# Kernel optimization log

Hardware: AMD Instinct MI355X
Metric: run time of the kernel (lower is better)

## Reference

```python
import jax, jax.numpy as jnp
import numpy as np

B, L, IN_DIM, D, NL, DI, DS, DC, DTR, V, TRM_LOOPS = 4, 2048, 480, 512, 8, 1024, 16, 4, 32, 21, 4
EPS = 1e-5


def _ln(x, g, b):
    mu = jnp.mean(x, axis=-1, keepdims=True)
    var = jnp.mean(jnp.square(x - mu), axis=-1, keepdims=True)
    return (x - mu) * jax.lax.rsqrt(var + EPS) * g + b


def setup_inputs() -> dict:
    key = jax.random.key(0)
    ks = iter(jax.random.split(key, 48))
    n = lambda shape, s=0.02: jax.random.normal(next(ks), shape, jnp.float32) * s
    return dict(
        x=jax.random.normal(next(ks), (B, L, IN_DIM), jnp.float32),
        enc_w1=n((D, IN_DIM)), enc_b1=jnp.zeros((D,), jnp.float32),
        enc_w2=n((D, D)), enc_b2=jnp.zeros((D,), jnp.float32),
        enc_g=jnp.ones((D,), jnp.float32), enc_beta=jnp.zeros((D,), jnp.float32),
        gru_wih=n((3 * D, D)), gru_whh=n((3 * D, D)),
        gru_bih=jnp.zeros((3 * D,), jnp.float32), gru_bhh=jnp.zeros((3 * D,), jnp.float32),
        prj_w1=n((D, D)), prj_b1=jnp.zeros((D,), jnp.float32),
        prj_w2=n((D, D)), prj_b2=jnp.zeros((D,), jnp.float32),
        trm_g=jnp.ones((D,), jnp.float32), trm_beta=jnp.zeros((D,), jnp.float32),
        in_w=n((NL, 2 * DI, D)),
        conv_w=n((NL, DI, 1, DC), 0.2), conv_b=jnp.zeros((NL, DI), jnp.float32),
        xproj_w=n((NL, DTR + 2 * DS, DI)),
        dt_w=n((NL, DI, DTR), 0.1), dt_b=n((NL, DI), 0.1),
        A_log=jnp.log(jnp.broadcast_to(jnp.arange(1, DS + 1, dtype=jnp.float32), (NL, DI, DS))),
        Dp=jnp.ones((NL, DI), jnp.float32),
        out_w=n((NL, D, DI)),
        ln_g=jnp.ones((NL, D), jnp.float32), ln_b=jnp.zeros((NL, D), jnp.float32),
        head_w=n((V, D)), head_b=jnp.zeros((V,), jnp.float32),
    )


def _mamba(x, in_w, conv_w, conv_b, xproj_w, dt_w, dt_b, A_log, Dp, out_w):
    # x: [B,L,D]
    xz = jnp.einsum('bld,ed->ble', x, in_w)          # [B,L,2*DI]
    xi, zgate = jnp.split(xz, 2, axis=-1)
    # depthwise causal conv over time
    xc = jnp.transpose(xi, (0, 2, 1))                # [B,DI,L]
    xc = jax.lax.conv_general_dilated(
        xc, conv_w, (1,), [(DC - 1, 0)], feature_group_count=DI,
        dimension_numbers=('NCH', 'OIH', 'NCH'))
    xc = jax.nn.silu(jnp.transpose(xc, (0, 2, 1)) + conv_b)   # [B,L,DI]
    dbl = jnp.einsum('bld,ed->ble', xc, xproj_w)     # [B,L,DTR+2*DS]
    dt = dbl[..., :DTR]
    Bm = dbl[..., DTR:DTR + DS]
    Cm = dbl[..., DTR + DS:]
    dt = jax.nn.softplus(jnp.einsum('blr,dr->bld', dt, dt_w) + dt_b)  # [B,L,DI]
    A = -jnp.exp(A_log)                              # [DI,DS]

    def step(h, ins):
        dt_t, B_t, C_t, x_t = ins                    # [B,DI],[B,DS],[B,DS],[B,DI]
        dA = jnp.exp(dt_t[:, :, None] * A)           # [B,DI,DS]
        h = dA * h + (dt_t * x_t)[:, :, None] * B_t[:, None, :]
        y = jnp.einsum('bds,bs->bd', h, C_t)
        return h, y

    h0 = jnp.zeros((x.shape[0], DI, DS), x.dtype)
    xs = (jnp.swapaxes(dt, 0, 1), jnp.swapaxes(Bm, 0, 1),
          jnp.swapaxes(Cm, 0, 1), jnp.swapaxes(xc, 0, 1))
    _, ys = jax.lax.scan(step, h0, xs)               # ys: [L,B,DI]
    y = jnp.swapaxes(ys, 0, 1) + xc * Dp
    y = y * jax.nn.silu(zgate)
    return jnp.einsum('ble,de->bld', y, out_w)


def reference(x, enc_w1, enc_b1, enc_w2, enc_b2, enc_g, enc_beta,
              gru_wih, gru_whh, gru_bih, gru_bhh,
              prj_w1, prj_b1, prj_w2, prj_b2, trm_g, trm_beta,
              in_w, conv_w, conv_b, xproj_w, dt_w, dt_b, A_log, Dp, out_w,
              ln_g, ln_b, head_w, head_b):
    # encoder
    h = jax.nn.gelu(x @ enc_w1.T + enc_b1, approximate=False)
    h = _ln(h @ enc_w2.T + enc_b2, enc_g, enc_beta)
    # TRM refinement
    b, l, d = h.shape
    xf = h.reshape(-1, d)
    z = jnp.zeros_like(xf)
    for _ in range(TRM_LOOPS):
        gi = xf @ gru_wih.T + gru_bih
        gh = z @ gru_whh.T + gru_bhh
        ir, iz, inn = jnp.split(gi, 3, axis=-1)
        hr, hz, hn = jnp.split(gh, 3, axis=-1)
        r = jax.nn.sigmoid(ir + hr)
        u = jax.nn.sigmoid(iz + hz)
        nn_ = jnp.tanh(inn + r * hn)
        z = (1.0 - u) * nn_ + u * z
        delta = jax.nn.gelu(z @ prj_w1.T + prj_b1, approximate=False) @ prj_w2.T + prj_b2
        xf = xf + delta
    h = _ln(xf, trm_g, trm_beta).reshape(b, l, d)
    # stacked Mamba blocks with post-norm residual
    for i in range(NL):
        h = _ln(h + _mamba(h, in_w[i], conv_w[i], conv_b[i], xproj_w[i],
                           dt_w[i], dt_b[i], A_log[i], Dp[i], out_w[i]),
                ln_g[i], ln_b[i])
    return h @ head_w.T + head_b
```

## Files before the change

kernel.cpp:

```cpp
#include <hip/hip_runtime.h>
#include <hip/hip_bf16.h>
#include <math.h>

#define BB 4
#define LL 2048
#define IN_DIM 480
#define DD 512
#define NLAYER 8
#define DI 1024
#define DS 16
#define DC 4
#define DTR 32
#define VV 21
#define TRM_LOOPS 4
#define ROWS (BB*LL)
#define EPSLN 1e-5f

#define NCHUNK 128
#define CLEN (LL / NCHUNK)

#define ACT_NONE 0
#define ACT_GELU 1
#define ACT_SOFTPLUS 2

typedef __attribute__((ext_vector_type(8))) short short8v;
typedef __attribute__((ext_vector_type(4))) float f32x4;

__device__ __forceinline__ float softplus_fast(float x) {
  return (x > 20.f) ? x : __logf(1.f + __expf(x));
}
__device__ __forceinline__ float bf2f(__hip_bfloat16 v) { return __bfloat162float(v); }

template<int ACT, bool RES, bool WF32, bool WBF16>
__global__ __launch_bounds__(256)
void gemm_mfma_bt(const __hip_bfloat16* __restrict__ A,
                  const __hip_bfloat16* __restrict__ B,
                  const float* __restrict__ bias,
                  const float* __restrict__ res,
                  float* __restrict__ Cf, __hip_bfloat16* __restrict__ Cb,
                  int M, int N, int K) {
  __shared__ short As[128 * 32];
  __shared__ short Bs[128 * 32];
  const int tid = threadIdx.x;
  const int lane = tid & 63;
  const int wv = tid >> 6;
  const int wr = (wv >> 1) * 64;
  const int wc = (wv & 1) * 64;
  const int fr = lane & 15;
  const int ko = (lane >> 4) * 8;

  int bid = blockIdx.y * gridDim.x + blockIdx.x;
  const int nwg = gridDim.x * gridDim.y;
  if ((nwg & 7) == 0) {
    bid = (bid & 7) * (nwg >> 3) + (bid >> 3);
  }
  const int m0 = (bid / gridDim.x) * 128;
  const int n0 = (bid % gridDim.x) * 128;

  f32x4 acc[4][4];
  #pragma unroll
  for (int i = 0; i < 4; ++i)
    #pragma unroll
    for (int j = 0; j < 4; ++j)
      acc[i][j] = (f32x4){0.f, 0.f, 0.f, 0.f};

  for (int k0 = 0; k0 < K; k0 += 32) {
    #pragma unroll
    for (int jj = 0; jj < 2; ++jj) {
      const int chunk = jj * 256 + tid;
      const int r = chunk >> 2;
      const int cb = (chunk & 3) * 8;
      const __hip_bfloat16* ga = A + (size_t)(m0 + r) * K + k0 + cb;
      __builtin_amdgcn_global_load_lds(
          (const __attribute__((address_space(1))) unsigned int*)ga,
          (__attribute__((address_space(3))) unsigned int*)&As[chunk * 8], 16, 0, 0);
      const __hip_bfloat16* gb = B + (size_t)(n0 + r) * K + k0 + cb;
      __builtin_amdgcn_global_load_lds(
          (const __attribute__((address_space(1))) unsigned int*)gb,
          (__attribute__((address_space(3))) unsigned int*)&Bs[chunk * 8], 16, 0, 0);
    }
    __syncthreads();

    short8v a[4], b[4];
    #pragma unroll
    for (int i = 0; i < 4; ++i)
      a[i] = *(const short8v*)&As[(wr + i * 16 + fr) * 32 + ko];
    #pragma unroll
    for (int j = 0; j < 4; ++j)
      b[j] = *(const short8v*)&Bs[(wc + j * 16 + fr) * 32 + ko];
    #pragma unroll
    for (int i = 0; i < 4; ++i)
      #pragma unroll
      for (int j = 0; j < 4; ++j)
        acc[i][j] = __builtin_amdgcn_mfma_f32_16x16x32_bf16(a[i], b[j], acc[i][j], 0, 0, 0);
    __syncthreads();
  }

  float bj[4];
  #pragma unroll
  for (int j = 0; j < 4; ++j)
    bj[j] = bias ? bias[n0 + wc + j * 16 + fr] : 0.f;
  const int r0 = (lane >> 4) * 4;
  #pragma unroll
  for (int i = 0; i < 4; ++i) {
    #pragma unroll
    for (int r = 0; r < 4; ++r) {
      const int row = m0 + wr + i * 16 + r0 + r;
      const size_t rb = (size_t)row * N;
      #pragma unroll
      for (int j = 0; j < 4; ++j) {
        const int col = n0 + wc + j * 16 + fr;
        float v = acc[i][j][r] + bj[j];
        if (ACT == ACT_GELU) v = 0.5f * v * (1.0f + erff(v * 0.70710678118654752f));
        if (ACT == ACT_SOFTPLUS) v = softplus_fast(v);
        if (RES) v += res[rb + col];
        if (WF32) Cf[rb + col] = v;
        if (WBF16) Cb[rb + col] = __float2bfloat16(v);
      }
    }
  }
}

template<bool ATOMIC, bool BIASF>
__global__ __launch_bounds__(256)
void gemm_mfma_n64(const __hip_bfloat16* __restrict__ A,
                   const __hip_bfloat16* __restrict__ B,
                   const float* __restrict__ bias,
                   float* __restrict__ C,
                   int M, int K, int klen, int nout, int ldc) {
  __shared__ short As[64 * 32];
  __shared__ short Bs[64 * 32];
  const int tid = threadIdx.x;
  const int lane = tid & 63;
  const int wv = tid >> 6;
  const int wr = (wv >> 1) * 32;
  const int wc = (wv & 1) * 32;
  const int fr = lane & 15;
  const int ko = (lane >> 4) * 8;
  const int m0 = blockIdx.y * 64;
  const int kbase = blockIdx.x * klen;

  f32x4 acc[2][2];
  #pragma unroll
  for (int i = 0; i < 2; ++i)
    #pragma unroll
    for (int j = 0; j < 2; ++j)
      acc[i][j] = (f32x4){0.f, 0.f, 0.f, 0.f};

  for (int k0 = kbase; k0 < kbase + klen; k0 += 32) {
    const int r = tid >> 2;
    const int cb = (tid & 3) * 8;
    const __hip_bfloat16* ga = A + (size_t)(m0 + r) * K + k0 + cb;
    __builtin_amdgcn_global_load_lds(
        (const __attribute__((address_space(1))) unsigned int*)ga,
        (__attribute__((address_space(3))) unsigned int*)&As[tid * 8], 16, 0, 0);
    const __hip_bfloat16* gb = B + (size_t)r * K + k0 + cb;
    __builtin_amdgcn_global_load_lds(
        (const __attribute__((address_space(1))) unsigned int*)gb,
        (__attribute__((address_space(3))) unsigned int*)&Bs[tid * 8], 16, 0, 0);
    __syncthreads();

    short8v a[2], b[2];
    #pragma unroll
    for (int i = 0; i < 2; ++i)
      a[i] = *(const short8v*)&As[(wr + i * 16 + fr) * 32 + ko];
    #pragma unroll
    for (int j = 0; j < 2; ++j)
      b[j] = *(const short8v*)&Bs[(wc + j * 16 + fr) * 32 + ko];
    #pragma unroll
    for (int i = 0; i < 2; ++i)
      #pragma unroll
      for (int j = 0; j < 2; ++j)
        acc[i][j] = __builtin_amdgcn_mfma_f32_16x16x32_bf16(a[i], b[j], acc[i][j], 0, 0, 0);
    __syncthreads();
  }

  const int r0 = (lane >> 4) * 4;
  #pragma unroll
  for (int i = 0; i < 2; ++i) {
    #pragma unroll
    for (int r = 0; r < 4; ++r) {
      const int row = m0 + wr + i * 16 + r0 + r;
      const size_t rb = (size_t)row * ldc;
      #pragma unroll
      for (int j = 0; j < 2; ++j) {
        const int col = wc + j * 16 + fr;
        float v = acc[i][j][r];
        if (ATOMIC) {
          atomicAdd(&C[rb + col], v);
        } else {
          if (col < nout) {
            if (BIASF) v += bias[col];
            C[rb + col] = v;
          }
        }
      }
    }
  }
}

__global__ __launch_bounds__(256)
void cvt_f2b(const float* __restrict__ s, __hip_bfloat16* __restrict__ d, int n) {
  int i = (blockIdx.x * 256 + threadIdx.x) * 4;
  if (i >= n) return;
  float4 v = *(const float4*)(s + i);
  d[i + 0] = __float2bfloat16(v.x);
  d[i + 1] = __float2bfloat16(v.y);
  d[i + 2] = __float2bfloat16(v.z);
  d[i + 3] = __float2bfloat16(v.w);
}

__global__ __launch_bounds__(256)
void cvt_dbl32(const float* __restrict__ dbl, __hip_bfloat16* __restrict__ o) {
  int i = blockIdx.x * 256 + threadIdx.x;
  if (i >= ROWS * 8) return;
  int row = i >> 3, q = (i & 7) * 4;
  float4 v = *(const float4*)(dbl + (size_t)row * 64 + q);
  short4 p;
  short* pp = (short*)&p;
  __hip_bfloat16 b0 = __float2bfloat16(v.x); pp[0] = *(short*)&b0;
  __hip_bfloat16 b1 = __float2bfloat16(v.y); pp[1] = *(short*)&b1;
  __hip_bfloat16 b2 = __float2bfloat16(v.z); pp[2] = *(short*)&b2;
  __hip_bfloat16 b3 = __float2bfloat16(v.w); pp[3] = *(short*)&b3;
  *(short4*)(o + (size_t)row * 32 + q) = p;
}

template<bool XF32>
__global__ __launch_bounds__(256)
void ln_kernel(const void* __restrict__ xv, const float* __restrict__ res,
               const float* __restrict__ g, const float* __restrict__ b,
               float* __restrict__ outf, __hip_bfloat16* __restrict__ outb) {
  const int row = blockIdx.x;
  const int t = threadIdx.x;
  const size_t base = (size_t)row * DD;
  float v0, v1;
  if (XF32) {
    const float* x = (const float*)xv;
    v0 = x[base + t]; v1 = x[base + t + 256];
  } else {
    const __hip_bfloat16* x = (const __hip_bfloat16*)xv;
    v0 = bf2f(x[base + t]); v1 = bf2f(x[base + t + 256]);
  }
  if (res) { v0 += res[base + t]; v1 += res[base + t + 256]; }
  float s  = v0 + v1;
  float ss = v0 * v0 + v1 * v1;
  #pragma unroll
  for (int off = 32; off > 0; off >>= 1) {
    s  += __shfl_down(s, off);
    ss += __shfl_down(ss, off);
  }
  __shared__ float red[2][4];
  int wave = t >> 6, lane = t & 63;
  if (lane == 0) { red[0][wave] = s; red[1][wave] = ss; }
  __syncthreads();
  if (t == 0) {
    float S = red[0][0] + red[0][1] + red[0][2] + red[0][3];
    float SS = red[1][0] + red[1][1] + red[1][2] + red[1][3];
    red[0][0] = S; red[1][0] = SS;
  }
  __syncthreads();
  float mean = red[0][0] * (1.f / DD);
  float var  = red[1][0] * (1.f / DD) - mean * mean;
  float inv  = rsqrtf(var + EPSLN);
  float o0 = (v0 - mean) * inv * g[t]       + b[t];
  float o1 = (v1 - mean) * inv * g[t + 256] + b[t + 256];
  outf[base + t]       = o0;
  outf[base + t + 256] = o1;
  outb[base + t]       = __float2bfloat16(o0);
  outb[base + t + 256] = __float2bfloat16(o1);
}

__device__ __forceinline__ float fsig(float x) { return 1.f / (1.f + __expf(-x)); }
__device__ __forceinline__ void bf4_load(const __hip_bfloat16* p, float* f) {
  short4 v = *(const short4*)p;
  f[0] = __uint_as_float(((unsigned)(unsigned short)v.x) << 16);
  f[1] = __uint_as_float(((unsigned)(unsigned short)v.y) << 16);
  f[2] = __uint_as_float(((unsigned)(unsigned short)v.z) << 16);
  f[3] = __uint_as_float(((unsigned)(unsigned short)v.w) << 16);
}

__global__ __launch_bounds__(256)
void gru_gates(const __hip_bfloat16* __restrict__ gi, const __hip_bfloat16* __restrict__ gh,
               float* __restrict__ z, __hip_bfloat16* __restrict__ zbf) {
  int idx4 = blockIdx.x * 256 + threadIdx.x;
  if (idx4 >= ROWS * DD / 4) return;
  const int m = idx4 >> 7;
  const int n = (idx4 & 127) * 4;
  const size_t base = (size_t)m * (3 * DD);
  float ir[4], iz[4], in_[4], hr[4], hz[4], hn[4];
  bf4_load(gi + base + n, ir);
  bf4_load(gi + base + 512 + n, iz);
  bf4_load(gi + base + 1024 + n, in_);
  bf4_load(gh + base + n, hr);
  bf4_load(gh + base + 512 + n, hz);
  bf4_load(gh + base + 1024 + n, hn);
  const size_t zo_i = (size_t)m * DD + n;
  float4 zov = *(const float4*)(z + zo_i);
  float zo[4] = {zov.x, zov.y, zov.z, zov.w};
  float zn[4];
  short4 ob;
  short* op = (short*)&ob;
  #pragma unroll
  for (int j = 0; j < 4; ++j) {
    float rg = fsig(ir[j] + hr[j]);
    float ug = fsig(iz[j] + hz[j]);
    float xx = in_[j] + rg * hn[j];
    xx = fminf(fmaxf(xx, -9.f), 9.f);
    float t2 = __expf(2.f * xx);
    float nn = (t2 - 1.f) / (t2 + 1.f);
    zn[j] = (1.f - ug) * nn + ug * zo[j];
    __hip_bfloat16 hb = __float2bfloat16(zn[j]);
    op[j] = *reinterpret_cast<short*>(&hb);
  }
  *(float4*)(z + zo_i) = make_float4(zn[0], zn[1], zn[2], zn[3]);
  *(short4*)(zbf + zo_i) = ob;
}

__global__ __launch_bounds__(256)
void conv_silu(const __hip_bfloat16* __restrict__ xz, const float* __restrict__ w,
               const float* __restrict__ cb, __hip_bfloat16* __restrict__ xc) {
  int idx4 = blockIdx.x * 256 + threadIdx.x;
  if (idx4 >= ROWS * DI / 4) return;
  const int d0 = (idx4 << 2) & (DI - 1);
  const int bl = idx4 >> 8;
  const int l = bl & (LL - 1);
  const __hip_bfloat16* xp = xz + (size_t)bl * (2 * DI) + d0;
  float t0[4] = {0,0,0,0}, t1[4] = {0,0,0,0}, t2[4] = {0,0,0,0}, t3[4];
  bf4_load(xp, t3);
  if (l >= 1) bf4_load(xp - (ptrdiff_t)(1 * 2 * DI), t2);
  if (l >= 2) bf4_load(xp - (ptrdiff_t)(2 * 2 * DI), t1);
  if (l >= 3) bf4_load(xp - (ptrdiff_t)(3 * 2 * DI), t0);
  float4 cbv = *(const float4*)(cb + d0);
  float cb4[4] = {cbv.x, cbv.y, cbv.z, cbv.w};
  short4 o;
  short* op = (short*)&o;
  #pragma unroll
  for (int j = 0; j < 4; ++j) {
    float4 wv = *(const float4*)(w + (d0 + j) * 4);
    float acc = cb4[j];
    acc = fmaf(wv.x, t0[j], acc);
    acc = fmaf(wv.y, t1[j], acc);
    acc = fmaf(wv.z, t2[j], acc);
    acc = fmaf(wv.w, t3[j], acc);
    float r = acc / (1.f + __expf(-acc));
    __hip_bfloat16 hb = __float2bfloat16(r);
    op[j] = *reinterpret_cast<short*>(&hb);
  }
  *(short4*)(xc + (size_t)bl * DI + d0) = o;
}


__global__ __launch_bounds__(256)
void scan_pass1(const __hip_bfloat16* __restrict__ xc, const float* __restrict__ dbl,
                const float* __restrict__ A_log, const __hip_bfloat16* __restrict__ dt,
                __hip_bfloat16* __restrict__ hF, float* __restrict__ dtsum) {
  __shared__ float sB[CLEN][DS];
  const int tid = threadIdx.x;
  const int d = (blockIdx.x & 3) * 256 + tid;
  const int c = (blockIdx.x >> 2) & (NCHUNK - 1);
  const int b = (int)(blockIdx.x >> 9);
  const size_t row0 = (size_t)b * LL + (size_t)c * CLEN;
  if (tid < CLEN * DS / 4) {
    const int r = tid >> 2, q = (tid & 3) * 4;
    float4 v = *(const float4*)(dbl + (row0 + r) * 64 + DTR + q);
    *(float4*)&sB[r][q] = v;
  }
  __syncthreads();

  const float A0 = -__expf(A_log[(size_t)d * DS]);
  float h[DS];
  #pragma unroll
  for (int s = 0; s < DS; ++s) h[s] = 0.f;
  float dts = 0.f;

  for (int l = 0; l < CLEN; ++l) {
    const size_t rk = row0 + l;
    float dtv = bf2f(dt[rk * DI + d]);
    dts += dtv;
    float xv = bf2f(xc[rk * DI + d]);
    float du = dtv * xv;
    float e1 = __expf(dtv * A0);
    float a = 1.f;
    #pragma unroll
    for (int s4 = 0; s4 < DS; s4 += 4) {
      float4 Bv = *(const float4*)&sB[l][s4];
      a *= e1; h[s4+0] = fmaf(a, h[s4+0], du * Bv.x);
      a *= e1; h[s4+1] = fmaf(a, h[s4+1], du * Bv.y);
      a *= e1; h[s4+2] = fmaf(a, h[s4+2], du * Bv.z);
      a *= e1; h[s4+3] = fmaf(a, h[s4+3], du * Bv.w);
    }
  }
  const size_t o = ((size_t)(b * NCHUNK + c) * DI + d) * DS;
  short4 pk[4];
  #pragma unroll
  for (int s4 = 0; s4 < DS; s4 += 4) {
    short* pp = (short*)&pk[s4 >> 2];
    #pragma unroll
    for (int j = 0; j < 4; ++j) {
      __hip_bfloat16 hb = __float2bfloat16(h[s4 + j]);
      pp[j] = *reinterpret_cast<short*>(&hb);
    }
    *(short4*)(hF + o + s4) = pk[s4 >> 2];
  }
  dtsum[(size_t)(b * NCHUNK + c) * DI + d] = dts;
}

__global__ __launch_bounds__(256)
void scan_pass2(const float* __restrict__ A_log, const float* __restrict__ dtsum,
                __hip_bfloat16* __restrict__ hF) {
  const int idx = blockIdx.x * 256 + threadIdx.x;
  const int s = idx & (DS - 1);
  const int d = (idx >> 4) & (DI - 1);
  const int b = idx >> 14;
  const float A = -__expf(A_log[d * DS + s]);
  float h = 0.f;
  for (int c = 0; c < NCHUNK; ++c) {
    const size_t cb = (size_t)(b * NCHUNK + c) * DI + d;
    const float p = __expf(dtsum[cb] * A);
    const size_t o = cb * DS + s;
    const float hf = bf2f(hF[o]);
    hF[o] = __float2bfloat16(h);
    h = fmaf(p, h, hf);
  }
}

__global__ __launch_bounds__(256)
void scan_pass3(const __hip_bfloat16* __restrict__ xc, const float* __restrict__ dbl,
                const float* __restrict__ A_log, const __hip_bfloat16* __restrict__ dt,
                const __hip_bfloat16* __restrict__ hin, const __hip_bfloat16* __restrict__ xz,
                const float* __restrict__ Dp, __hip_bfloat16* __restrict__ y) {
  __shared__ float sbc[CLEN][32];
  const int tid = threadIdx.x;
  const int d = (blockIdx.x & 3) * 256 + tid;
  const int c = (blockIdx.x >> 2) & (NCHUNK - 1);
  const int b = (int)(blockIdx.x >> 9);
  const size_t row0 = (size_t)b * LL + (size_t)c * CLEN;
  if (tid < CLEN * 32 / 4) {
    const int r = tid >> 3, q = (tid & 7) * 4;
    float4 v = *(const float4*)(dbl + (row0 + r) * 64 + DTR + q);
    *(float4*)&sbc[r][q] = v;
  }
  __syncthreads();

  const float A0 = -__expf(A_log[(size_t)d * DS]);
  float h[DS];
  const size_t o = ((size_t)(b * NCHUNK + c) * DI + d) * DS;
  #pragma unroll
  for (int s4 = 0; s4 < DS; s4 += 4) {
    float hv[4];
    bf4_load(hin + o + s4, hv);
    h[s4] = hv[0]; h[s4+1] = hv[1]; h[s4+2] = hv[2]; h[s4+3] = hv[3];
  }
  const float Dval = Dp[d];

  for (int l = 0; l < CLEN; ++l) {
    const size_t rk = row0 + l;
    float dtv = bf2f(dt[rk * DI + d]);
    float xv = bf2f(xc[rk * DI + d]);
    float du = dtv * xv;
    float e1 = __expf(dtv * A0);
    float a = 1.f;
    float acc = 0.f;
    #pragma unroll
    for (int s4 = 0; s4 < DS; s4 += 4) {
      float4 Bv = *(const float4*)&sbc[l][s4];
      float4 Cv = *(const float4*)&sbc[l][16 + s4];
      a *= e1; h[s4+0] = fmaf(a, h[s4+0], du * Bv.x); acc = fmaf(h[s4+0], Cv.x, acc);
      a *= e1; h[s4+1] = fmaf(a, h[s4+1], du * Bv.y); acc = fmaf(h[s4+1], Cv.y, acc);
      a *= e1; h[s4+2] = fmaf(a, h[s4+2], du * Bv.z); acc = fmaf(h[s4+2], Cv.z, acc);
      a *= e1; h[s4+3] = fmaf(a, h[s4+3], du * Bv.w); acc = fmaf(h[s4+3], Cv.w, acc);
    }
    float zg = bf2f(xz[rk * 2 * DI + DI + d]);
    float sz = zg / (1.f + __expf(-zg));
    y[rk * DI + d] = __float2bfloat16(fmaf(xv, Dval, acc) * sz);
  }
}

extern "C" void kernel_launch(void* const* d_in, const int* in_sizes, int n_in,
                              void* d_out, int out_size, void* d_ws, size_t ws_size,
                              hipStream_t stream) {
  (void)in_sizes; (void)n_in; (void)out_size; (void)ws_size;
  const float* x       = (const float*)d_in[0];
  const float* enc_w1  = (const float*)d_in[1];
  const float* enc_b1  = (const float*)d_in[2];
  const float* enc_w2  = (const float*)d_in[3];
  const float* enc_b2  = (const float*)d_in[4];
  const float* enc_g   = (const float*)d_in[5];
  const float* enc_beta= (const float*)d_in[6];
  const float* gru_wih = (const float*)d_in[7];
  const float* gru_whh = (const float*)d_in[8];
  const float* gru_bih = (const float*)d_in[9];
  const float* gru_bhh = (const float*)d_in[10];
  const float* prj_w1  = (const float*)d_in[11];
  const float* prj_b1  = (const float*)d_in[12];
  const float* prj_w2  = (const float*)d_in[13];
  const float* prj_b2  = (const float*)d_in[14];
  const float* trm_g   = (const float*)d_in[15];
  const float* trm_beta= (const float*)d_in[16];
  const float* in_w    = (const float*)d_in[17];
  const float* conv_w  = (const float*)d_in[18];
  const float* conv_b  = (const float*)d_in[19];
  const float* xproj_w = (const float*)d_in[20];
  const float* dt_w    = (const float*)d_in[21];
  const float* dt_b    = (const float*)d_in[22];
  const float* A_log   = (const float*)d_in[23];
  const float* Dp      = (const float*)d_in[24];
  const float* out_w   = (const float*)d_in[25];
  const float* ln_g    = (const float*)d_in[26];
  const float* ln_b    = (const float*)d_in[27];
  const float* head_w  = (const float*)d_in[28];
  const float* head_b  = (const float*)d_in[29];
  float* out = (float*)d_out;

  float* ws = (float*)d_ws;
  float* h     = ws + 0;
  __hip_bfloat16* hbf   = (__hip_bfloat16*)(ws + 4194304);
  __hip_bfloat16* wenc1 = (__hip_bfloat16*)(ws + 6291456);
  __hip_bfloat16* wenc2 = (__hip_bfloat16*)(ws + 6414336);
  __hip_bfloat16* wgih  = (__hip_bfloat16*)(ws + 6545408);
  __hip_bfloat16* wghh  = (__hip_bfloat16*)(ws + 6938624);
  __hip_bfloat16* wp1   = (__hip_bfloat16*)(ws + 7331840);
  __hip_bfloat16* wp2   = (__hip_bfloat16*)(ws + 7462912);
  __hip_bfloat16* win   = (__hip_bfloat16*)(ws + 7593984);
  __hip_bfloat16* wout  = (__hip_bfloat16*)(ws + 11788288);
  __hip_bfloat16* wxp   = (__hip_bfloat16*)(ws + 13885440);
  __hip_bfloat16* whead = (__hip_bfloat16*)(ws + 14147584);
  __hip_bfloat16* wdtb  = (__hip_bfloat16*)(ws + 14163968);
  float* p0 = ws + 14295040;
  __hip_bfloat16* tmpb2 = (__hip_bfloat16*)p0;
  __hip_bfloat16* xbf   = (__hip_bfloat16*)(p0 + 4194304);
  __hip_bfloat16* tmpbf = (__hip_bfloat16*)(p0 + 31457280);
  float* z  = p0;
  __hip_bfloat16* zbf = (__hip_bfloat16*)(p0 + 4194304);
  __hip_bfloat16* gib = (__hip_bfloat16*)(p0 + 6291456);
  __hip_bfloat16* ghb = (__hip_bfloat16*)(p0 + 12582912);
  __hip_bfloat16* xzbf = (__hip_bfloat16*)p0;
  __hip_bfloat16* xcbf = (__hip_bfloat16*)(p0 + 8388608);
  float* dbl = p0 + 12582912;
  __hip_bfloat16* ybbf = (__hip_bfloat16*)(p0 + 13107200);
  __hip_bfloat16* hFb  = (__hip_bfloat16*)(p0 + 17301504);
  float* dts = p0 + 21495808;
  __hip_bfloat16* dtb16 = (__hip_bfloat16*)(p0 + 22020096);
  __hip_bfloat16* dblb  = (__hip_bfloat16*)(p0 + 26214400);
  __hip_bfloat16* tmpob = (__hip_bfloat16*)(p0 + 26345472);

  dim3 b256(256);
  dim3 gG((ROWS * DD / 4 + 255) / 256), gLN(ROWS);
  dim3 gConv((ROWS * DI / 4 + 255) / 256);
  dim3 gScan(BB * NCHUNK * (DI / 256));
  dim3 gScan2(BB * DI * DS / 256);

  {
    auto cvt = [&](const float* s, __hip_bfloat16* d, int n) {
      hipLaunchKernelGGL(cvt_f2b, dim3((n / 4 + 255) / 256), b256, 0, stream, s, d, n);
    };
    cvt(x, xbf, ROWS * IN_DIM);
    cvt(enc_w1, wenc1, DD * IN_DIM);
    cvt(enc_w2, wenc2, DD * DD);
    cvt(gru_wih, wgih, 3 * DD * DD);
    cvt(gru_whh, wghh, 3 * DD * DD);
    cvt(prj_w1, wp1, DD * DD);
    cvt(prj_w2, wp2, DD * DD);
    cvt(in_w, win, NLAYER * 2 * DI * DD);
    cvt(out_w, wout, NLAYER * DD * DI);
    cvt(xproj_w, wxp, NLAYER * 64 * DI);
    cvt(dt_w, wdtb, NLAYER * DI * DTR);
    hipMemsetAsync(whead, 0, 64 * DD * sizeof(__hip_bfloat16), stream);
    cvt(head_w, whead, VV * DD);
  }

  hipLaunchKernelGGL((gemm_mfma_bt<ACT_GELU, false, false, true>), dim3(DD/128, ROWS/128), b256, 0, stream,
                     xbf, wenc1, enc_b1, nullptr, nullptr, tmpbf, ROWS, DD, IN_DIM);
  hipLaunchKernelGGL((gemm_mfma_bt<ACT_NONE, false, false, true>), dim3(DD/128, ROWS/128), b256, 0, stream,
                     tmpbf, wenc2, enc_b2, nullptr, nullptr, tmpb2, ROWS, DD, DD);
  hipLaunchKernelGGL((ln_kernel<false>), gLN, b256, 0, stream, tmpb2, (const float*)nullptr, enc_g, enc_beta, h, hbf);

  hipMemsetAsync(z, 0, (size_t)ROWS * DD * sizeof(float), stream);
  hipMemsetAsync(zbf, 0, (size_t)ROWS * DD * sizeof(__hip_bfloat16), stream);
  for (int it = 0; it < TRM_LOOPS; ++it) {
    hipLaunchKernelGGL((gemm_mfma_bt<ACT_NONE, false, false, true>), dim3(3*DD/128, ROWS/128), b256, 0, stream,
                       hbf, wgih, gru_bih, nullptr, nullptr, gib, ROWS, 3 * DD, DD);
    hipLaunchKernelGGL((gemm_mfma_bt<ACT_NONE, false, false, true>), dim3(3*DD/128, ROWS/128), b256, 0, stream,
                       zbf, wghh, gru_bhh, nullptr, nullptr, ghb, ROWS, 3 * DD, DD);
    hipLaunchKernelGGL(gru_gates, gG, b256, 0, stream, gib, ghb, z, zbf);
    hipLaunchKernelGGL((gemm_mfma_bt<ACT_GELU, false, false, true>), dim3(DD/128, ROWS/128), b256, 0, stream,
                       zbf, wp1, prj_b1, nullptr, nullptr, tmpbf, ROWS, DD, DD);
    hipLaunchKernelGGL((gemm_mfma_bt<ACT_NONE, true, true, true>), dim3(DD/128, ROWS/128), b256, 0, stream,
                       tmpbf, wp2, prj_b2, h, h, hbf, ROWS, DD, DD);
  }
  hipLaunchKernelGGL((ln_kernel<true>), gLN, b256, 0, stream, h, (const float*)nullptr, trm_g, trm_beta, h, hbf);

  for (int i = 0; i < NLAYER; ++i) {
    const __hip_bfloat16* iw  = win  + (size_t)i * 2 * DI * DD;
    const __hip_bfloat16* ow  = wout + (size_t)i * DD * DI;
    const __hip_bfloat16* xpw = wxp  + (size_t)i * 64 * DI;
    const __hip_bfloat16* dwb = wdtb + (size_t)i * DI * DTR;
    const float* cw  = conv_w  + (size_t)i * DI * DC;
    const float* cbi = conv_b  + (size_t)i * DI;
    const float* db  = dt_b    + (size_t)i * DI;
    const float* Al  = A_log   + (size_t)i * DI * DS;
    const float* Dpi = Dp      + (size_t)i * DI;
    const float* lgi = ln_g    + (size_t)i * DD;
    const float* lbi = ln_b    + (size_t)i * DD;

    hipLaunchKernelGGL((gemm_mfma_bt<ACT_NONE, false, false, true>), dim3(2*DI/128, ROWS/128), b256, 0, stream,
                       hbf, iw, nullptr, nullptr, nullptr, xzbf, ROWS, 2 * DI, DD);
    hipLaunchKernelGGL(conv_silu, gConv, b256, 0, stream, xzbf, cw, cbi, xcbf);
    hipMemsetAsync(dbl, 0, (size_t)ROWS * 64 * sizeof(float), stream);
    hipLaunchKernelGGL((gemm_mfma_n64<true, false>), dim3(2, ROWS / 64), b256, 0, stream,
                       xcbf, xpw, nullptr, dbl, ROWS, DI, DI / 2, 64, 64);
    hipLaunchKernelGGL(cvt_dbl32, dim3(ROWS * 8 / 256), b256, 0, stream, dbl, dblb);
    hipLaunchKernelGGL((gemm_mfma_bt<ACT_SOFTPLUS, false, false, true>), dim3(DI/128, ROWS/128), b256, 0, stream,
                       dblb, dwb, db, nullptr, nullptr, dtb16, ROWS, DI, DTR);
    hipLaunchKernelGGL(scan_pass1, gScan, b256, 0, stream, xcbf, dbl, Al, dtb16, hFb, dts);
    hipLaunchKernelGGL(scan_pass2, gScan2, b256, 0, stream, Al, dts, hFb);
    hipLaunchKernelGGL(scan_pass3, gScan, b256, 0, stream, xcbf, dbl, Al, dtb16, hFb, xzbf, Dpi, ybbf);
    hipLaunchKernelGGL((gemm_mfma_bt<ACT_NONE, false, false, true>), dim3(DD/128, ROWS/128), b256, 0, stream,
                       ybbf, ow, nullptr, nullptr, nullptr, tmpob, ROWS, DD, DI);
    hipLaunchKernelGGL((ln_kernel<false>), gLN, b256, 0, stream, tmpob, h, lgi, lbi, h, hbf);
  }

  hipLaunchKernelGGL((gemm_mfma_n64<false, true>), dim3(1, ROWS / 64), b256, 0, stream,
                     hbf, whead, head_b, out, ROWS, DD, DD, VV, VV);
}
```

Measured before the change: 1.818 ms.

## Skip first GRU hidden GEMM, fuse dbl zeroing, prefetch scan loads

On the first TRM iteration z is zero, so the hidden-state GEMM is replaced by loading the bias directly in a specialised gru_gates kernel. The fp32 z buffer is dropped and the recurrent state is kept only in bf16, which removes the memsets and the fp32 traffic but rounds the GRU state each iteration. The per-layer memset of dbl is folded into conv_silu. The scan kernels software-prefetch the next row's x, dt and gate values to hide load latency.

```diff
diff --git a/kernel.cpp b/kernel.cpp
--- a/kernel.cpp
+++ b/kernel.cpp
@@ -279,9 +279,10 @@
   f[3] = __uint_as_float(((unsigned)(unsigned short)v.w) << 16);
 }
 
+template<bool FIRST>
 __global__ __launch_bounds__(256)
 void gru_gates(const __hip_bfloat16* __restrict__ gi, const __hip_bfloat16* __restrict__ gh,
-               float* __restrict__ z, __hip_bfloat16* __restrict__ zbf) {
+               const float* __restrict__ bhh, __hip_bfloat16* __restrict__ zbf) {
   int idx4 = blockIdx.x * 256 + threadIdx.x;
   if (idx4 >= ROWS * DD / 4) return;
   const int m = idx4 >> 7;
@@ -291,13 +292,21 @@
   bf4_load(gi + base + n, ir);
   bf4_load(gi + base + 512 + n, iz);
   bf4_load(gi + base + 1024 + n, in_);
-  bf4_load(gh + base + n, hr);
-  bf4_load(gh + base + 512 + n, hz);
-  bf4_load(gh + base + 1024 + n, hn);
+  if (FIRST) {
+    float4 a = *(const float4*)(bhh + n);
+    float4 bq = *(const float4*)(bhh + 512 + n);
+    float4 cq = *(const float4*)(bhh + 1024 + n);
+    hr[0]=a.x; hr[1]=a.y; hr[2]=a.z; hr[3]=a.w;
+    hz[0]=bq.x; hz[1]=bq.y; hz[2]=bq.z; hz[3]=bq.w;
+    hn[0]=cq.x; hn[1]=cq.y; hn[2]=cq.z; hn[3]=cq.w;
+  } else {
+    bf4_load(gh + base + n, hr);
+    bf4_load(gh + base + 512 + n, hz);
+    bf4_load(gh + base + 1024 + n, hn);
+  }
   const size_t zo_i = (size_t)m * DD + n;
-  float4 zov = *(const float4*)(z + zo_i);
-  float zo[4] = {zov.x, zov.y, zov.z, zov.w};
-  float zn[4];
+  float zo[4] = {0.f, 0.f, 0.f, 0.f};
+  if (!FIRST) bf4_load(zbf + zo_i, zo);
   short4 ob;
   short* op = (short*)&ob;
   #pragma unroll
@@ -308,19 +317,22 @@
     xx = fminf(fmaxf(xx, -9.f), 9.f);
     float t2 = __expf(2.f * xx);
     float nn = (t2 - 1.f) / (t2 + 1.f);
-    zn[j] = (1.f - ug) * nn + ug * zo[j];
-    __hip_bfloat16 hb = __float2bfloat16(zn[j]);
+    float zn = FIRST ? (1.f - ug) * nn : ((1.f - ug) * nn + ug * zo[j]);
+    __hip_bfloat16 hb = __float2bfloat16(zn);
     op[j] = *reinterpret_cast<short*>(&hb);
   }
-  *(float4*)(z + zo_i) = make_float4(zn[0], zn[1], zn[2], zn[3]);
   *(short4*)(zbf + zo_i) = ob;
 }
 
 __global__ __launch_bounds__(256)
 void conv_silu(const __hip_bfloat16* __restrict__ xz, const float* __restrict__ w,
-               const float* __restrict__ cb, __hip_bfloat16* __restrict__ xc) {
+               const float* __restrict__ cb, __hip_bfloat16* __restrict__ xc,
+               float* __restrict__ dbl_zero) {
   int idx4 = blockIdx.x * 256 + threadIdx.x;
   if (idx4 >= ROWS * DI / 4) return;
+  if (idx4 < ROWS * 64 / 4) {
+    *(float4*)(dbl_zero + (size_t)idx4 * 4) = make_float4(0.f, 0.f, 0.f, 0.f);
+  }
   const int d0 = (idx4 << 2) & (DI - 1);
   const int bl = idx4 >> 8;
   const int l = bl & (LL - 1);
@@ -373,11 +385,18 @@
   for (int s = 0; s < DS; ++s) h[s] = 0.f;
   float dts = 0.f;
 
+  const __hip_bfloat16* xp = xc + row0 * DI + d;
+  const __hip_bfloat16* dp = dt + row0 * DI + d;
+  float xv_n = bf2f(xp[0]);
+  float dt_n = bf2f(dp[0]);
+  #pragma unroll 4
   for (int l = 0; l < CLEN; ++l) {
-    const size_t rk = row0 + l;
-    float dtv = bf2f(dt[rk * DI + d]);
+    float xv = xv_n, dtv = dt_n;
+    if (l + 1 < CLEN) {
+      xv_n = bf2f(xp[(size_t)(l + 1) * DI]);
+      dt_n = bf2f(dp[(size_t)(l + 1) * DI]);
+    }
     dts += dtv;
-    float xv = bf2f(xc[rk * DI + d]);
     float du = dtv * xv;
     float e1 = __expf(dtv * A0);
     float a = 1.f;
@@ -391,16 +410,16 @@
     }
   }
   const size_t o = ((size_t)(b * NCHUNK + c) * DI + d) * DS;
-  short4 pk[4];
   #pragma unroll
   for (int s4 = 0; s4 < DS; s4 += 4) {
-    short* pp = (short*)&pk[s4 >> 2];
+    short4 pk;
+    short* pp = (short*)&pk;
     #pragma unroll
     for (int j = 0; j < 4; ++j) {
       __hip_bfloat16 hb = __float2bfloat16(h[s4 + j]);
       pp[j] = *reinterpret_cast<short*>(&hb);
     }
-    *(short4*)(hF + o + s4) = pk[s4 >> 2];
+    *(short4*)(hF + o + s4) = pk;
   }
   dtsum[(size_t)(b * NCHUNK + c) * DI + d] = dts;
 }
@@ -414,13 +433,21 @@
   const int b = idx >> 14;
   const float A = -__expf(A_log[d * DS + s]);
   float h = 0.f;
+  size_t cb = (size_t)b * NCHUNK * DI + d;
+  float dts_n = dtsum[cb];
+  float hf_n = bf2f(hF[cb * DS + s]);
   for (int c = 0; c < NCHUNK; ++c) {
-    const size_t cb = (size_t)(b * NCHUNK + c) * DI + d;
-    const float p = __expf(dtsum[cb] * A);
+    const float dtsv = dts_n;
+    const float hf = hf_n;
     const size_t o = cb * DS + s;
-    const float hf = bf2f(hF[o]);
+    if (c + 1 < NCHUNK) {
+      dts_n = dtsum[cb + DI];
+      hf_n = bf2f(hF[(cb + DI) * DS + s]);
+    }
+    const float p = __expf(dtsv * A);
     hF[o] = __float2bfloat16(h);
     h = fmaf(p, h, hf);
+    cb += DI;
   }
 }
 
@@ -453,10 +480,21 @@
   }
   const float Dval = Dp[d];
 
+  const __hip_bfloat16* xp = xc + row0 * DI + d;
+  const __hip_bfloat16* dp = dt + row0 * DI + d;
+  const __hip_bfloat16* zp = xz + row0 * 2 * DI + DI + d;
+  float xv_n = bf2f(xp[0]);
+  float dt_n = bf2f(dp[0]);
+  float zg_n = bf2f(zp[0]);
+  #pragma unroll 4
   for (int l = 0; l < CLEN; ++l) {
     const size_t rk = row0 + l;
-    float dtv = bf2f(dt[rk * DI + d]);
-    float xv = bf2f(xc[rk * DI + d]);
+    float xv = xv_n, dtv = dt_n, zg = zg_n;
+    if (l + 1 < CLEN) {
+      xv_n = bf2f(xp[(size_t)(l + 1) * DI]);
+      dt_n = bf2f(dp[(size_t)(l + 1) * DI]);
+      zg_n = bf2f(zp[(size_t)(l + 1) * 2 * DI]);
+    }
     float du = dtv * xv;
     float e1 = __expf(dtv * A0);
     float a = 1.f;
@@ -470,7 +508,6 @@
       a *= e1; h[s4+2] = fmaf(a, h[s4+2], du * Bv.z); acc = fmaf(h[s4+2], Cv.z, acc);
       a *= e1; h[s4+3] = fmaf(a, h[s4+3], du * Bv.w); acc = fmaf(h[s4+3], Cv.w, acc);
     }
-    float zg = bf2f(xz[rk * 2 * DI + DI + d]);
     float sz = zg / (1.f + __expf(-zg));
     y[rk * DI + d] = __float2bfloat16(fmaf(xv, Dval, acc) * sz);
   }
@@ -530,10 +567,9 @@
   __hip_bfloat16* tmpb2 = (__hip_bfloat16*)p0;
   __hip_bfloat16* xbf   = (__hip_bfloat16*)(p0 + 4194304);
   __hip_bfloat16* tmpbf = (__hip_bfloat16*)(p0 + 31457280);
-  float* z  = p0;
-  __hip_bfloat16* zbf = (__hip_bfloat16*)(p0 + 4194304);
-  __hip_bfloat16* gib = (__hip_bfloat16*)(p0 + 6291456);
-  __hip_bfloat16* ghb = (__hip_bfloat16*)(p0 + 12582912);
+  __hip_bfloat16* zbf = (__hip_bfloat16*)p0;
+  __hip_bfloat16* gib = (__hip_bfloat16*)(p0 + 2097152);
+  __hip_bfloat16* ghb = (__hip_bfloat16*)(p0 + 8388608);
   __hip_bfloat16* xzbf = (__hip_bfloat16*)p0;
   __hip_bfloat16* xcbf = (__hip_bfloat16*)(p0 + 8388608);
   float* dbl = p0 + 12582912;
@@ -575,14 +611,16 @@
                      tmpbf, wenc2, enc_b2, nullptr, nullptr, tmpb2, ROWS, DD, DD);
   hipLaunchKernelGGL((ln_kernel<false>), gLN, b256, 0, stream, tmpb2, (const float*)nullptr, enc_g, enc_beta, h, hbf);
 
-  hipMemsetAsync(z, 0, (size_t)ROWS * DD * sizeof(float), stream);
-  hipMemsetAsync(zbf, 0, (size_t)ROWS * DD * sizeof(__hip_bfloat16), stream);
   for (int it = 0; it < TRM_LOOPS; ++it) {
     hipLaunchKernelGGL((gemm_mfma_bt<ACT_NONE, false, false, true>), dim3(3*DD/128, ROWS/128), b256, 0, stream,
                        hbf, wgih, gru_bih, nullptr, nullptr, gib, ROWS, 3 * DD, DD);
-    hipLaunchKernelGGL((gemm_mfma_bt<ACT_NONE, false, false, true>), dim3(3*DD/128, ROWS/128), b256, 0, stream,
-                       zbf, wghh, gru_bhh, nullptr, nullptr, ghb, ROWS, 3 * DD, DD);
-    hipLaunchKernelGGL(gru_gates, gG, b256, 0, stream, gib, ghb, z, zbf);
+    if (it == 0) {
+      hipLaunchKernelGGL((gru_gates<true>), gG, b256, 0, stream, gib, ghb, gru_bhh, zbf);
+    } else {
+      hipLaunchKernelGGL((gemm_mfma_bt<ACT_NONE, false, false, true>), dim3(3*DD/128, ROWS/128), b256, 0, stream,
+                         zbf, wghh, gru_bhh, nullptr, nullptr, ghb, ROWS, 3 * DD, DD);
+      hipLaunchKernelGGL((gru_gates<false>), gG, b256, 0, stream, gib, ghb, gru_bhh, zbf);
+    }
     hipLaunchKernelGGL((gemm_mfma_bt<ACT_GELU, false, false, true>), dim3(DD/128, ROWS/128), b256, 0, stream,
                        zbf, wp1, prj_b1, nullptr, nullptr, tmpbf, ROWS, DD, DD);
     hipLaunchKernelGGL((gemm_mfma_bt<ACT_NONE, true, true, true>), dim3(DD/128, ROWS/128), b256, 0, stream,
@@ -605,8 +643,7 @@
 
     hipLaunchKernelGGL((gemm_mfma_bt<ACT_NONE, false, false, true>), dim3(2*DI/128, ROWS/128), b256, 0, stream,
                        hbf, iw, nullptr, nullptr, nullptr, xzbf, ROWS, 2 * DI, DD);
-    hipLaunchKernelGGL(conv_silu, gConv, b256, 0, stream, xzbf, cw, cbi, xcbf);
-    hipMemsetAsync(dbl, 0, (size_t)ROWS * 64 * sizeof(float), stream);
+    hipLaunchKernelGGL(conv_silu, gConv, b256, 0, stream, xzbf, cw, cbi, xcbf, dbl);
     hipLaunchKernelGGL((gemm_mfma_n64<true, false>), dim3(2, ROWS / 64), b256, 0, stream,
                        xcbf, xpw, nullptr, dbl, ROWS, DI, DI / 2, 64, 64);
     hipLaunchKernelGGL(cvt_dbl32, dim3(ROWS * 8 / 256), b256, 0, stream, dbl, dblb);
```

After: 1.783 ms. Within noise of the previous version (-1.9%).
